# Kernel optimization log

Hardware: AMD Instinct MI355X
Metric: run time of the kernel (lower is better)

## Reference

```python
import jax, jax.numpy as jnp
import numpy as np

W_MODE, W_COMFORT, W_PROGRESS, W_COLLISION, W_DRIVABLE = 1.0, 0.1, 0.5, 1.0, 0.3
COLLISION_RADIUS = 2.0
LANE_MAX_DIST = 3.0
BIG = 1000000.0


def setup_inputs() -> dict:
    key = jax.random.key(0)
    k1, k2, k3, k4 = jax.random.split(key, 4)
    B, M, T = 16, 60, 80
    N_AGENTS, N_LANES, N_PTS = 128, 64, 20
    return {
        "mode_logits": jax.random.normal(k1, (B, M), dtype=jnp.float32),
        "all_trajs": jax.random.normal(k2, (B, M, T, 3), dtype=jnp.float32),
        "agents_now": jax.random.normal(k3, (B, N_AGENTS, 4), dtype=jnp.float32),
        "agents_mask": jnp.ones((B, N_AGENTS), dtype=jnp.float32),
        "map_lanes": jax.random.normal(k4, (B, N_LANES, N_PTS, 3), dtype=jnp.float32),
        "map_lanes_mask": jnp.ones((B, N_LANES), dtype=jnp.float32),
    }


def reference(mode_logits, all_trajs, agents_now, agents_mask, map_lanes, map_lanes_mask):
    B, M, T, _ = all_trajs.shape
    mode_scores = jax.nn.softmax(mode_logits, axis=-1)  # (B, M)

    ego_xy = all_trajs[..., :2]  # (B, M, T, 2)

    # Comfort: mean jerk norm (3rd finite difference of position)
    vel = ego_xy[:, :, 1:] - ego_xy[:, :, :-1]
    acc = vel[:, :, 1:] - vel[:, :, :-1]
    jerk = acc[:, :, 1:] - acc[:, :, :-1]
    comfort = -jnp.linalg.norm(jerk, axis=-1).mean(axis=-1)  # (B, M)

    # Progress: final x-coordinate
    progress = all_trajs[:, :, -1, 0]  # (B, M)

    # Collision: fraction of timesteps within radius of any valid agent
    agent_xy = agents_now[:, :, :2]  # (B, N, 2)
    # (B, M, T, N): pairwise distance ego trajectory points vs agents
    d_ag = jnp.linalg.norm(ego_xy[:, :, :, None, :] - agent_xy[:, None, None, :, :], axis=-1)
    d_ag = d_ag + (1.0 - agents_mask[:, None, None, :]) * BIG
    min_dist = d_ag.min(axis=-1)  # (B, M, T)
    collision = -(min_dist < COLLISION_RADIUS).astype(jnp.float32).mean(axis=-1)  # (B, M)

    # Drivable: fraction of timesteps farther than lane_max_dist from any valid lane point
    B_, L, P, _ = map_lanes.shape
    lane_flat = map_lanes[..., :2].reshape(B, L * P, 2)  # (B, L*P, 2)
    lane_valid_flat = jnp.repeat(map_lanes_mask, P, axis=1)  # (B, L*P)
    d_ln = jnp.linalg.norm(ego_xy[:, :, :, None, :] - lane_flat[:, None, None, :, :], axis=-1)
    d_ln = d_ln + (1.0 - lane_valid_flat[:, None, None, :]) * BIG
    min_lane_dist = d_ln.min(axis=-1)  # (B, M, T)
    drivable = -(min_lane_dist > LANE_MAX_DIST).astype(jnp.float32).mean(axis=-1)  # (B, M)

    score = (W_MODE * mode_scores + W_COMFORT * comfort + W_PROGRESS * progress
             + W_COLLISION * collision + W_DRIVABLE * drivable)  # (B, M)
    selected_idx = jnp.argmax(score, axis=1)  # (B,)
    selected_traj = all_trajs[jnp.arange(B), selected_idx]  # (B, T, 3)
    return selected_traj, selected_idx
```

## Files before the change

### kernel.cpp

```cpp
#include <hip/hip_runtime.h>
#include <math.h>

#define BM 60
#define TT 80
#define NAG 128
#define NLANES 64
#define NPTS 20
#define NLP (NLANES * NPTS)
#define PPL (NLP / 64)
#define APL (NAG / 64)

__global__ __launch_bounds__(64) void score_kernel(
    const float* __restrict__ trajs,
    const float* __restrict__ agents,
    const float* __restrict__ amask,
    const float* __restrict__ lanes,
    const float* __restrict__ lmask,
    float* __restrict__ scores)
{
    __shared__ float s_ex[TT], s_ey[TT];

    const int bm   = blockIdx.x;
    const int b    = bm / BM;
    const int lane = threadIdx.x;

    const float* tr = trajs + (size_t)bm * TT * 3;

    for (int i = lane; i < TT; i += 64) {
        s_ex[i] = tr[i * 3 + 0];
        s_ey[i] = tr[i * 3 + 1];
    }

    float ax[APL], ay[APL];
#pragma unroll
    for (int k = 0; k < APL; ++k) {
        const int i = lane + 64 * k;
        const float off = (1.0f - amask[b * NAG + i]) * 1e8f;
        ax[k] = agents[((size_t)b * NAG + i) * 4 + 0] + off;
        ay[k] = agents[((size_t)b * NAG + i) * 4 + 1];
    }
    float px[PPL], py[PPL];
#pragma unroll
    for (int k = 0; k < PPL; ++k) {
        const int i = lane + 64 * k;
        const float off = (1.0f - lmask[b * NLANES + i / NPTS]) * 1e8f;
        px[k] = lanes[((size_t)b * NLP + i) * 3 + 0] + off;
        py[k] = lanes[((size_t)b * NLP + i) * 3 + 1];
    }

    __syncthreads();

    int ccoll = 0, cdriv = 0;
    for (int r = 0; r < TT / 8; ++r) {
        float ex[8], ey[8], m2[8], m3[8];
#pragma unroll
        for (int j = 0; j < 8; ++j) {
            ex[j] = s_ex[r * 8 + j];
            ey[j] = s_ey[r * 8 + j];
            m2[j] = 1e30f;
            m3[j] = 1e30f;
        }
#pragma unroll
        for (int k = 0; k < APL; ++k) {
#pragma unroll
            for (int j = 0; j < 8; ++j) {
                const float dx = ex[j] - ax[k];
                const float dy = ey[j] - ay[k];
                m2[j] = fminf(m2[j], fmaf(dx, dx, dy * dy));
            }
        }
#pragma unroll
        for (int k = 0; k < PPL; ++k) {
#pragma unroll
            for (int j = 0; j < 8; ++j) {
                const float dx = ex[j] - px[k];
                const float dy = ey[j] - py[k];
                m3[j] = fminf(m3[j], fmaf(dx, dx, dy * dy));
            }
        }
#pragma unroll
        for (int j = 0; j < 8; ++j) {
            ccoll += (__ballot(m2[j] < 4.0f) != 0ull) ? 1 : 0;
            cdriv += (__ballot(m3[j] <= 9.0f) == 0ull) ? 1 : 0;
        }
    }

    float jsum = 0.0f;
    if (lane < TT - 3) {
        const float jx = s_ex[lane + 3] - 3.0f * s_ex[lane + 2] + 3.0f * s_ex[lane + 1] - s_ex[lane];
        const float jy = s_ey[lane + 3] - 3.0f * s_ey[lane + 2] + 3.0f * s_ey[lane + 1] - s_ey[lane];
        jsum = sqrtf(jx * jx + jy * jy);
    }
    {
        const int t2 = lane + 64;
        if (t2 < TT - 3) {
            const float jx = s_ex[t2 + 3] - 3.0f * s_ex[t2 + 2] + 3.0f * s_ex[t2 + 1] - s_ex[t2];
            const float jy = s_ey[t2 + 3] - 3.0f * s_ey[t2 + 2] + 3.0f * s_ey[t2 + 1] - s_ey[t2];
            jsum += sqrtf(jx * jx + jy * jy);
        }
    }
    for (int off = 32; off > 0; off >>= 1) jsum += __shfl_xor(jsum, off, 64);

    if (lane == 0) {
        const float comfort  = -(jsum / (float)(TT - 3));
        const float progress = tr[(TT - 1) * 3 + 0];
        scores[bm] = 0.1f * comfort + 0.5f * progress
                   - 1.0f * ((float)ccoll / (float)TT)
                   - 0.3f * ((float)cdriv / (float)TT);
    }
}

__global__ __launch_bounds__(64) void select_kernel(
    const float* __restrict__ logits,
    const float* __restrict__ trajs,
    const float* __restrict__ scores,
    float* __restrict__ out,
    int B)
{
    const int b    = blockIdx.x;
    const int lane = threadIdx.x;

    float lg = (lane < BM) ? logits[b * BM + lane] : -1e30f;
    float mx = lg;
    for (int off = 32; off > 0; off >>= 1) mx = fmaxf(mx, __shfl_xor(mx, off, 64));
    float e = (lane < BM) ? expf(lg - mx) : 0.0f;
    float sum = e;
    for (int off = 32; off > 0; off >>= 1) sum += __shfl_xor(sum, off, 64);

    float sc = (lane < BM) ? (e / sum + scores[b * BM + lane]) : -1e30f;
    int idx = lane;
    for (int off = 32; off > 0; off >>= 1) {
        float os = __shfl_xor(sc, off, 64);
        int   oi = __shfl_xor(idx, off, 64);
        if (os > sc || (os == sc && oi < idx)) { sc = os; idx = oi; }
    }
    const float* src = trajs + ((size_t)b * BM + idx) * TT * 3;
    for (int k = lane; k < TT * 3; k += 64) out[b * TT * 3 + k] = src[k];
    if (lane == 0) out[B * TT * 3 + b] = (float)idx;
}

extern "C" void kernel_launch(void* const* d_in, const int* in_sizes, int n_in,
                              void* d_out, int out_size, void* d_ws, size_t ws_size,
                              hipStream_t stream) {
    const float* logits = (const float*)d_in[0];
    const float* trajs  = (const float*)d_in[1];
    const float* agents = (const float*)d_in[2];
    const float* amask  = (const float*)d_in[3];
    const float* lanes  = (const float*)d_in[4];
    const float* lmask  = (const float*)d_in[5];

    const int B = in_sizes[0] / BM;
    float* scores = (float*)d_ws;
    float* out    = (float*)d_out;

    score_kernel<<<B * BM, 64, 0, stream>>>(trajs, agents, amask, lanes, lmask, scores);
    select_kernel<<<B, 64, 0, stream>>>(logits, trajs, scores, out, B);
}
```

Before: 84.80 us.

## Expand squared distance algebraically and split timesteps across two wavefronts

```diff
diff --git a/kernel.cpp b/kernel.cpp
--- a/kernel.cpp
+++ b/kernel.cpp
@@ -10,7 +10,7 @@
 #define PPL (NLP / 64)
 #define APL (NAG / 64)
 
-__global__ __launch_bounds__(64) void score_kernel(
+__global__ __launch_bounds__(128) void score_kernel(
     const float* __restrict__ trajs,
     const float* __restrict__ agents,
     const float* __restrict__ amask,
@@ -19,44 +19,66 @@
     float* __restrict__ scores)
 {
     __shared__ float s_ex[TT], s_ey[TT];
+    __shared__ float s_jerk;
+    __shared__ float s_cc[2], s_cd[2];
 
     const int bm   = blockIdx.x;
     const int b    = bm / BM;
-    const int lane = threadIdx.x;
+    const int tid  = threadIdx.x;
+    const int w    = tid >> 6;
+    const int lane = tid & 63;
 
     const float* tr = trajs + (size_t)bm * TT * 3;
-
-    for (int i = lane; i < TT; i += 64) {
+    for (int i = tid; i < TT; i += 128) {
         s_ex[i] = tr[i * 3 + 0];
         s_ey[i] = tr[i * 3 + 1];
     }
+    if (tid == 0) s_jerk = 0.0f;
 
-    float ax[APL], ay[APL];
+    float ax[APL], ay[APL], aq[APL];
 #pragma unroll
     for (int k = 0; k < APL; ++k) {
         const int i = lane + 64 * k;
         const float off = (1.0f - amask[b * NAG + i]) * 1e8f;
-        ax[k] = agents[((size_t)b * NAG + i) * 4 + 0] + off;
-        ay[k] = agents[((size_t)b * NAG + i) * 4 + 1];
+        const float x = agents[((size_t)b * NAG + i) * 4 + 0] + off;
+        const float y = agents[((size_t)b * NAG + i) * 4 + 1];
+        ax[k] = x; ay[k] = y; aq[k] = fmaf(x, x, y * y);
     }
-    float px[PPL], py[PPL];
+    float px[PPL], py[PPL], pq[PPL];
 #pragma unroll
     for (int k = 0; k < PPL; ++k) {
         const int i = lane + 64 * k;
         const float off = (1.0f - lmask[b * NLANES + i / NPTS]) * 1e8f;
-        px[k] = lanes[((size_t)b * NLP + i) * 3 + 0] + off;
-        py[k] = lanes[((size_t)b * NLP + i) * 3 + 1];
+        const float x = lanes[((size_t)b * NLP + i) * 3 + 0] + off;
+        const float y = lanes[((size_t)b * NLP + i) * 3 + 1];
+        px[k] = x; py[k] = y; pq[k] = fmaf(x, x, y * y);
     }
 
     __syncthreads();
 
+    float jsum = 0.0f;
+    if (tid < TT - 3) {
+        const float jx = s_ex[tid + 3] - 3.0f * s_ex[tid + 2] + 3.0f * s_ex[tid + 1] - s_ex[tid];
+        const float jy = s_ey[tid + 3] - 3.0f * s_ey[tid + 2] + 3.0f * s_ey[tid + 1] - s_ey[tid];
+        jsum = sqrtf(jx * jx + jy * jy);
+    }
+    for (int off = 32; off > 0; off >>= 1) jsum += __shfl_xor(jsum, off, 64);
+    if (lane == 0 && jsum != 0.0f) atomicAdd(&s_jerk, jsum);
+    if (lane == 0 && jsum == 0.0f) atomicAdd(&s_jerk, 0.0f);
+
     int ccoll = 0, cdriv = 0;
-    for (int r = 0; r < TT / 8; ++r) {
-        float ex[8], ey[8], m2[8], m3[8];
+    const int t0 = w * (TT / 2);
+    for (int r = 0; r < (TT / 2) / 8; ++r) {
+        float mx8[8], my8[8], thrA[8], thrB[8], m2[8], m3[8];
 #pragma unroll
         for (int j = 0; j < 8; ++j) {
-            ex[j] = s_ex[r * 8 + j];
-            ey[j] = s_ey[r * 8 + j];
+            const float ex = s_ex[t0 + r * 8 + j];
+            const float ey = s_ey[t0 + r * 8 + j];
+            const float c  = fmaf(ex, ex, ey * ey);
+            mx8[j]  = -2.0f * ex;
+            my8[j]  = -2.0f * ey;
+            thrA[j] = 4.0f - c;
+            thrB[j] = 9.0f - c;
             m2[j] = 1e30f;
             m3[j] = 1e30f;
         }
@@ -64,49 +86,37 @@
         for (int k = 0; k < APL; ++k) {
 #pragma unroll
             for (int j = 0; j < 8; ++j) {
-                const float dx = ex[j] - ax[k];
-                const float dy = ey[j] - ay[k];
-                m2[j] = fminf(m2[j], fmaf(dx, dx, dy * dy));
+                float v = fmaf(my8[j], ay[k], aq[k]);
+                v = fmaf(mx8[j], ax[k], v);
+                m2[j] = fminf(m2[j], v);
             }
         }
 #pragma unroll
         for (int k = 0; k < PPL; ++k) {
 #pragma unroll
             for (int j = 0; j < 8; ++j) {
-                const float dx = ex[j] - px[k];
-                const float dy = ey[j] - py[k];
-                m3[j] = fminf(m3[j], fmaf(dx, dx, dy * dy));
+                float v = fmaf(my8[j], py[k], pq[k]);
+                v = fmaf(mx8[j], px[k], v);
+                m3[j] = fminf(m3[j], v);
             }
         }
 #pragma unroll
         for (int j = 0; j < 8; ++j) {
-            ccoll += (__ballot(m2[j] < 4.0f) != 0ull) ? 1 : 0;
-            cdriv += (__ballot(m3[j] <= 9.0f) == 0ull) ? 1 : 0;
+            ccoll += (__ballot(m2[j] < thrA[j]) != 0ull) ? 1 : 0;
+            cdriv += (__ballot(m3[j] <= thrB[j]) == 0ull) ? 1 : 0;
         }
     }
+    if (lane == 0) { s_cc[w] = (float)ccoll; s_cd[w] = (float)cdriv; }
+    __syncthreads();
 
-    float jsum = 0.0f;
-    if (lane < TT - 3) {
-        const float jx = s_ex[lane + 3] - 3.0f * s_ex[lane + 2] + 3.0f * s_ex[lane + 1] - s_ex[lane];
-        const float jy = s_ey[lane + 3] - 3.0f * s_ey[lane + 2] + 3.0f * s_ey[lane + 1] - s_ey[lane];
-        jsum = sqrtf(jx * jx + jy * jy);
-    }
-    {
-        const int t2 = lane + 64;
-        if (t2 < TT - 3) {
-            const float jx = s_ex[t2 + 3] - 3.0f * s_ex[t2 + 2] + 3.0f * s_ex[t2 + 1] - s_ex[t2];
-            const float jy = s_ey[t2 + 3] - 3.0f * s_ey[t2 + 2] + 3.0f * s_ey[t2 + 1] - s_ey[t2];
-            jsum += sqrtf(jx * jx + jy * jy);
-        }
-    }
-    for (int off = 32; off > 0; off >>= 1) jsum += __shfl_xor(jsum, off, 64);
-
-    if (lane == 0) {
-        const float comfort  = -(jsum / (float)(TT - 3));
+    if (tid == 0) {
+        const float coll = s_cc[0] + s_cc[1];
+        const float driv = s_cd[0] + s_cd[1];
+        const float comfort  = -(s_jerk / (float)(TT - 3));
         const float progress = tr[(TT - 1) * 3 + 0];
         scores[bm] = 0.1f * comfort + 0.5f * progress
-                   - 1.0f * ((float)ccoll / (float)TT)
-                   - 0.3f * ((float)cdriv / (float)TT);
+                   - 1.0f * (coll / (float)TT)
+                   - 0.3f * (driv / (float)TT);
     }
 }
 
@@ -153,6 +163,6 @@
     float* scores = (float*)d_ws;
     float* out    = (float*)d_out;
 
-    score_kernel<<<B * BM, 64, 0, stream>>>(trajs, agents, amask, lanes, lmask, scores);
+    score_kernel<<<B * BM, 128, 0, stream>>>(trajs, agents, amask, lanes, lmask, scores);
     select_kernel<<<B, 64, 0, stream>>>(logits, trajs, scores, out, B);
 }
```

Result: faster. 77.38 us (-8.7%).
